# Performance work log

Hardware: AMD Instinct MI355X
Metric: run time of the kernel (lower is better)

## Reference

```python
import jax, jax.numpy as jnp
import numpy as np

TOPK = 8            # args.topk
SWAP_RATIO = 0.3    # args.swap_ratio
NUM_SPECIAL = 999   # first non-special wordpiece id in bert-base-uncased


def setup_inputs() -> dict:
    key = jax.random.key(0)
    k0, k1, k2, k3, k4, k5 = jax.random.split(key, 6)
    B, S, V, D = 4, 512, 30522, 768
    return {
        "delta_grad": jax.random.normal(k0, (B, S, D), jnp.float32),
        "src_embeds": jax.random.normal(k1, (B, S, D), jnp.float32),
        "embedding_matrix": jax.random.normal(k2, (V, D), jnp.float32),
        "src_tokens": jax.random.randint(k3, (B, S), 0, V),
        "pred_lm": jax.random.normal(k4, (B, S, V), jnp.float32),
        "attention_mask": jnp.ones((B, S), jnp.int32),
        "rand_u": jax.random.uniform(k5, (B, S), jnp.float32),
    }


def reference(delta_grad, src_embeds, embedding_matrix, src_tokens, pred_lm, attention_mask, rand_u):
    B, S, D = delta_grad.shape
    V = embedding_matrix.shape[0]
    neg_inf = jnp.float32(-np.inf)

    # dir_dot_grad = -(prev_dot - new_dot) = new_dot - prev_dot
    new_dot = jnp.einsum('bsd,vd->bsv', delta_grad, embedding_matrix)   # [B,S,V]
    prev_dot = jnp.einsum('bsd,bsd->bs', delta_grad, src_embeds)        # [B,S]
    dir_dot_grad = new_dot - prev_dot[..., None]

    # pairwise euclidean distance between src_embeds and vocab embeddings
    src_sq = jnp.sum(src_embeds * src_embeds, axis=-1)                  # [B,S]
    vocab_sq = jnp.sum(embedding_matrix * embedding_matrix, axis=-1)    # [V]
    dot = jnp.einsum('bsd,vd->bsv', src_embeds, embedding_matrix)       # [B,S,V]
    sq_norm = src_sq[..., None] + vocab_sq[None, None, :] - 2.0 * dot
    dir_norm = jnp.sqrt(jax.nn.relu(sq_norm) + 1e-20)

    dir_dot_grad = dir_dot_grad / dir_norm

    # LM top-k allowed-token mask (scatter of 0 into a -inf mask in torch)
    _, topk_idx = jax.lax.top_k(pred_lm, TOPK)                          # [B,S,K]
    topk_idx = topk_idx * attention_mask[..., None].astype(topk_idx.dtype)
    bi = jnp.arange(B)[:, None, None]
    si = jnp.arange(S)[None, :, None]
    allowed = jnp.zeros((B, S, V), bool).at[bi, si, topk_idx].set(True)

    filtered = jnp.where(allowed, dir_dot_grad, neg_inf)
    # special tokens [:999] -> -inf (overrides any topk scatter there)
    filtered = jnp.where(jnp.arange(V)[None, None, :] < NUM_SPECIAL, neg_inf, filtered)
    # forbid keeping the original token
    filtered = jnp.where(jnp.arange(V)[None, None, :] == src_tokens[..., None], neg_inf, filtered)

    adv_flip = jnp.argmax(filtered, axis=2)                             # [B,S]

    # swap mask: non-special positions, Bernoulli(swap_ratio)
    no_special = src_tokens >= NUM_SPECIAL
    swap = rand_u > (1.0 - SWAP_RATIO)
    mask_idx = (no_special & swap).astype(src_tokens.dtype)

    adv_tokens = src_tokens * (1 - mask_idx) + adv_flip.astype(src_tokens.dtype) * mask_idx
    return adv_tokens
```

## Files before the change

### kernel.cpp

```cpp
#include <hip/hip_runtime.h>
#include <math.h>

constexpr int TOPK = 8;
constexpr int NUM_SPECIAL = 999;
constexpr int V = 30522;
constexpr int D = 768;
constexpr int BLOCK = 256;
constexpr int NCAND = BLOCK * TOPK;

__device__ __forceinline__ unsigned long long fkey(float v, unsigned int idx) {
    unsigned int u = __float_as_uint(v);
    u = ((int)u < 0) ? ~u : (u | 0x80000000u);
    return ((unsigned long long)u << 32) | (unsigned long long)(~idx);
}

__device__ __forceinline__ void ins8(unsigned long long (&loc)[TOPK],
                                     unsigned long long key) {
    if (key > loc[TOPK - 1]) {
        loc[TOPK - 1] = key;
        #pragma unroll
        for (int j = TOPK - 1; j > 0; --j) {
            unsigned long long a = loc[j - 1], b = loc[j];
            loc[j - 1] = a > b ? a : b;
            loc[j]     = a > b ? b : a;
        }
    }
}

__global__ __launch_bounds__(BLOCK) void dvat_kernel(
    const float* __restrict__ delta_grad,
    const float* __restrict__ src_embeds,
    const float* __restrict__ emb,
    const int*   __restrict__ src_tokens,
    const float* __restrict__ pred_lm,
    const int*   __restrict__ attn,
    const float* __restrict__ rand_u,
    int* __restrict__ out)
{
    const int pos = blockIdx.x;
    const int tid = threadIdx.x;
    const int lane = tid & 63;
    const int wave = tid >> 6;

    __shared__ unsigned long long sh[NCAND];
    __shared__ int    s_cand[TOPK];
    __shared__ double s_scores[TOPK];
    __shared__ double s_pd[4], s_ssq[4];

    const float* row = pred_lm + (size_t)pos * V;
    unsigned long long loc[TOPK];
    #pragma unroll
    for (int i = 0; i < TOPK; ++i) loc[i] = 0ull;

    const float2* row2 = (const float2*)row;
    constexpr int V2 = V / 2;
    for (int i = tid; i < V2; i += BLOCK) {
        float2 f = row2[i];
        unsigned int base = (unsigned int)(i * 2);
        ins8(loc, fkey(f.x, base));
        ins8(loc, fkey(f.y, base + 1));
    }

    #pragma unroll
    for (int j = 0; j < TOPK; ++j) sh[tid * TOPK + j] = loc[j];
    __syncthreads();

    for (int it = 0; it < TOPK; ++it) {
        if (tid < 64) {
            unsigned long long m = 0ull;
            int ml = 0;
            for (int j = tid; j < NCAND; j += 64) {
                unsigned long long x = sh[j];
                if (x > m) { m = x; ml = j; }
            }
            #pragma unroll
            for (int off = 32; off; off >>= 1) {
                unsigned long long om = __shfl_down(m, off, 64);
                int ol = __shfl_down(ml, off, 64);
                if (om > m) { m = om; ml = ol; }
            }
            if (tid == 0) {
                s_cand[it] = (int)(~(unsigned int)m);
                sh[ml] = 0ull;
            }
        }
        __syncthreads();
    }

    if (tid == 0 && attn[pos] == 0) {
        #pragma unroll
        for (int k = 0; k < TOPK; ++k) s_cand[k] = 0;
    }
    __syncthreads();

    float* shf = (float*)sh;
    const float* dg = delta_grad + (size_t)pos * D;
    const float* se = src_embeds + (size_t)pos * D;

    double pd = 0.0, ssq = 0.0;
    for (int i = tid; i < D; i += BLOCK) {
        float g = dg[i], e = se[i];
        shf[i] = g;
        shf[D + i] = e;
        pd  += (double)g * (double)e;
        ssq += (double)e * (double)e;
    }
    #pragma unroll
    for (int off = 32; off; off >>= 1) {
        pd  += __shfl_down(pd, off, 64);
        ssq += __shfl_down(ssq, off, 64);
    }
    if (lane == 0) { s_pd[wave] = pd; s_ssq[wave] = ssq; }
    __syncthreads();

    const double prev_dot = s_pd[0] + s_pd[1] + s_pd[2] + s_pd[3];
    const double src_sq   = s_ssq[0] + s_ssq[1] + s_ssq[2] + s_ssq[3];

    #pragma unroll
    for (int kk = 0; kk < 2; ++kk) {
        const int k = 2 * wave + kk;
        const int v = s_cand[k];
        const float* ev = emb + (size_t)v * D;
        double ddg = 0.0, dse = 0.0, dvv = 0.0;
        for (int i = lane; i < D; i += 64) {
            double e = (double)ev[i];
            ddg += e * (double)shf[i];
            dse += e * (double)shf[D + i];
            dvv += e * e;
        }
        #pragma unroll
        for (int off = 32; off; off >>= 1) {
            ddg += __shfl_down(ddg, off, 64);
            dse += __shfl_down(dse, off, 64);
            dvv += __shfl_down(dvv, off, 64);
        }
        if (lane == 0) {
            double sq = src_sq + dvv - 2.0 * dse;
            if (sq < 0.0) sq = 0.0;
            double dn = sqrt(sq + 1e-20);
            s_scores[k] = (ddg - prev_dot) / dn;
        }
    }
    __syncthreads();

    if (tid == 0) {
        const int src_tok = src_tokens[pos];
        int best = 0;
        double best_s = 0.0;
        bool found = false;
        #pragma unroll
        for (int k = 0; k < TOPK; ++k) {
            const int v = s_cand[k];
            if (v < NUM_SPECIAL || v == src_tok) continue;
            const double sc = s_scores[k];
            if (!found || sc > best_s || (sc == best_s && v < best)) {
                best = v; best_s = sc; found = true;
            }
        }
        const int adv_flip = found ? best : 0;
        const bool no_special = (src_tok >= NUM_SPECIAL);
        const bool swap = (rand_u[pos] > 0.7f);
        out[pos] = (no_special && swap) ? adv_flip : src_tok;
    }
}

extern "C" void kernel_launch(void* const* d_in, const int* in_sizes, int n_in,
                              void* d_out, int out_size, void* d_ws, size_t ws_size,
                              hipStream_t stream) {
    const float* delta_grad = (const float*)d_in[0];
    const float* src_embeds = (const float*)d_in[1];
    const float* emb        = (const float*)d_in[2];
    const int*   src_tokens = (const int*)d_in[3];
    const float* pred_lm    = (const float*)d_in[4];
    const int*   attn       = (const int*)d_in[5];
    const float* randu      = (const float*)d_in[6];
    int* out = (int*)d_out;

    const int BS = in_sizes[3];
    dvat_kernel<<<BS, BLOCK, 0, stream>>>(delta_grad, src_embeds, emb,
                                          src_tokens, pred_lm, attn, randu, out);
}
```

Measured before the change: 444.8 us.

## Replace keyed top-k insertion with value-only top-8 threshold and candidate recollection

The per-thread top-8 selection now tracks only float values in branchless min/max sorting networks (two independent lanes for the x/y halves), merges them in shared memory to find the 8th-largest value, then rescans the pred_lm row to collect every element at or above that threshold into a small candidate list with indices. The exact top-8 with tie-breaking is then chosen from that list. This removes the divergent 64-bit key insertion from the hot loop, at the cost of a second pass over the row (likely L2-resident) plus shared-memory atomics. The candidate list is capped, so heavy ties at the threshold could drop candidates.

Measured after the change: 457.5 us. +2.8%, slower.

```diff
diff --git a/kernel.cpp b/kernel.cpp
--- a/kernel.cpp
+++ b/kernel.cpp
@@ -1,30 +1,19 @@
 #include <hip/hip_runtime.h>
 #include <math.h>
+#include <float.h>
 
 constexpr int TOPK = 8;
 constexpr int NUM_SPECIAL = 999;
 constexpr int V = 30522;
 constexpr int D = 768;
 constexpr int BLOCK = 256;
-constexpr int NCAND = BLOCK * TOPK;
+constexpr int V2 = V / 2;
+constexpr int CAP = 512;
 
 __device__ __forceinline__ unsigned long long fkey(float v, unsigned int idx) {
     unsigned int u = __float_as_uint(v);
     u = ((int)u < 0) ? ~u : (u | 0x80000000u);
     return ((unsigned long long)u << 32) | (unsigned long long)(~idx);
-}
-
-__device__ __forceinline__ void ins8(unsigned long long (&loc)[TOPK],
-                                     unsigned long long key) {
-    if (key > loc[TOPK - 1]) {
-        loc[TOPK - 1] = key;
-        #pragma unroll
-        for (int j = TOPK - 1; j > 0; --j) {
-            unsigned long long a = loc[j - 1], b = loc[j];
-            loc[j - 1] = a > b ? a : b;
-            loc[j]     = a > b ? b : a;
-        }
-    }
 }
 
 __global__ __launch_bounds__(BLOCK) void dvat_kernel(
@@ -42,46 +31,95 @@
     const int lane = tid & 63;
     const int wave = tid >> 6;
 
-    __shared__ unsigned long long sh[NCAND];
+    __shared__ float sh_vals[BLOCK * TOPK];
+    __shared__ unsigned long long sh_cand64[CAP];
+    __shared__ int    s_ncand;
+    __shared__ float  s_g8;
     __shared__ int    s_cand[TOPK];
     __shared__ double s_scores[TOPK];
     __shared__ double s_pd[4], s_ssq[4];
 
-    const float* row = pred_lm + (size_t)pos * V;
-    unsigned long long loc[TOPK];
-    #pragma unroll
-    for (int i = 0; i < TOPK; ++i) loc[i] = 0ull;
-
-    const float2* row2 = (const float2*)row;
-    constexpr int V2 = V / 2;
+    const float2* row2 = (const float2*)(pred_lm + (size_t)pos * V);
+
+    float vx[TOPK], vy[TOPK];
+    #pragma unroll
+    for (int j = 0; j < TOPK; ++j) { vx[j] = -INFINITY; vy[j] = -INFINITY; }
+
     for (int i = tid; i < V2; i += BLOCK) {
         float2 f = row2[i];
-        unsigned int base = (unsigned int)(i * 2);
-        ins8(loc, fkey(f.x, base));
-        ins8(loc, fkey(f.y, base + 1));
-    }
-
-    #pragma unroll
-    for (int j = 0; j < TOPK; ++j) sh[tid * TOPK + j] = loc[j];
+        float t = f.x;
+        #pragma unroll
+        for (int j = 0; j < TOPK; ++j) {
+            float m = fmaxf(vx[j], t); t = fminf(vx[j], t); vx[j] = m;
+        }
+        t = f.y;
+        #pragma unroll
+        for (int j = 0; j < TOPK; ++j) {
+            float m = fmaxf(vy[j], t); t = fminf(vy[j], t); vy[j] = m;
+        }
+    }
+    float v8[TOPK];
+    #pragma unroll
+    for (int j = 0; j < TOPK; ++j) v8[j] = fmaxf(vx[j], vy[TOPK - 1 - j]);
+
+    #pragma unroll
+    for (int j = 0; j < TOPK; ++j) sh_vals[j * BLOCK + tid] = v8[j];
     __syncthreads();
 
     for (int it = 0; it < TOPK; ++it) {
         if (tid < 64) {
-            unsigned long long m = 0ull;
-            int ml = 0;
-            for (int j = tid; j < NCAND; j += 64) {
-                unsigned long long x = sh[j];
-                if (x > m) { m = x; ml = j; }
+            float m = -INFINITY; int ms = 0;
+            for (int j = tid; j < BLOCK * TOPK; j += 64) {
+                float x = sh_vals[j];
+                if (x > m) { m = x; ms = j; }
+            }
+            #pragma unroll
+            for (int off = 32; off; off >>= 1) {
+                float om = __shfl_down(m, off, 64);
+                int   os = __shfl_down(ms, off, 64);
+                if (om > m) { m = om; ms = os; }
+            }
+            if (tid == 0) {
+                sh_vals[ms] = -INFINITY;
+                if (it == TOPK - 1) s_g8 = m;
+            }
+        }
+        __syncthreads();
+    }
+
+    if (tid == 0) s_ncand = 0;
+    __syncthreads();
+    const float g8 = s_g8;
+    for (int i = tid; i < V2; i += BLOCK) {
+        float2 f = row2[i];
+        if (f.x >= g8) {
+            int p = atomicAdd(&s_ncand, 1);
+            if (p < CAP) sh_cand64[p] = fkey(f.x, (unsigned)(2 * i));
+        }
+        if (f.y >= g8) {
+            int p = atomicAdd(&s_ncand, 1);
+            if (p < CAP) sh_cand64[p] = fkey(f.y, (unsigned)(2 * i + 1));
+        }
+    }
+    __syncthreads();
+    const int ncand = min(s_ncand, CAP);
+
+    for (int it = 0; it < TOPK; ++it) {
+        if (tid < 64) {
+            unsigned long long m = 0ull; int ms = 0;
+            for (int j = tid; j < ncand; j += 64) {
+                unsigned long long x = sh_cand64[j];
+                if (x > m) { m = x; ms = j; }
             }
             #pragma unroll
             for (int off = 32; off; off >>= 1) {
                 unsigned long long om = __shfl_down(m, off, 64);
-                int ol = __shfl_down(ml, off, 64);
-                if (om > m) { m = om; ml = ol; }
+                int os = __shfl_down(ms, off, 64);
+                if (om > m) { m = om; ms = os; }
             }
             if (tid == 0) {
-                s_cand[it] = (int)(~(unsigned int)m);
-                sh[ml] = 0ull;
+                s_cand[it] = (m == 0ull) ? 0 : (int)(~(unsigned int)m);
+                sh_cand64[ms] = 0ull;
             }
         }
         __syncthreads();
@@ -93,7 +131,7 @@
     }
     __syncthreads();
 
-    float* shf = (float*)sh;
+    float* shf = sh_vals;
     const float* dg = delta_grad + (size_t)pos * D;
     const float* se = src_embeds + (size_t)pos * D;
 
```
